# Kernel tuning notes

Hardware: AMD Instinct MI355X
Metric: run time of the kernel (lower is better)

The kernel has to match this reference:

```python
import jax, jax.numpy as jnp
import numpy as np

EPS = 1e-5

def _ln(x, s, b):
    m = jnp.mean(x, axis=-1, keepdims=True)
    v = jnp.mean((x - m) ** 2, axis=-1, keepdims=True)
    return (x - m) * jax.lax.rsqrt(v + EPS) * s + b

def _lin(x, w, b):
    # torch nn.Linear: y = x @ w.T + b, w shape (out, in)
    return jnp.einsum('...i,oi->...o', x, w) + b

def _gelu(x):
    return jax.nn.gelu(x, approximate=False)  # torch nn.GELU default (erf)

def setup_inputs() -> dict:
    key = jax.random.key(0)
    L, B, N, P, D, F, H = 4, 16, 8, 64, 128, 128, 8
    ks = jax.random.split(key, 16)
    nrm = lambda k, s: jax.random.normal(k, s, jnp.float32) * 0.02
    return {
        'sequence': jax.random.normal(ks[0], (B, N, P, D), jnp.float32),
        'H_pre': jax.random.normal(ks[1], (L, B, N, P, D), jnp.float32),
        'pro1_w': nrm(ks[2], (L, F, D)), 'pro1_b': jnp.zeros((L, F), jnp.float32),
        'pro2_w': nrm(ks[3], (L, F, D)), 'pro2_b': jnp.zeros((L, F), jnp.float32),
        'ln_cur_s': jnp.ones((L, F), jnp.float32), 'ln_cur_b': jnp.zeros((L, F), jnp.float32),
        'ln_pre_s': jnp.ones((L, F), jnp.float32), 'ln_pre_b': jnp.zeros((L, F), jnp.float32),
        'cur_qkv_w': nrm(ks[4], (L, 3 * H * F, F)), 'cur_qkv_b': jnp.zeros((L, 3 * H * F), jnp.float32),
        'pre_qkv_w': nrm(ks[5], (L, 3 * H * F, F)), 'pre_qkv_b': jnp.zeros((L, 3 * H * F), jnp.float32),
        'alpha': jax.random.uniform(ks[6], (L, 3, H * F), jnp.float32),
        'proj_w': nrm(ks[7], (L, F, H * F)), 'proj_b': jnp.zeros((L, F), jnp.float32),
        'bn1_s': jnp.ones((L, F), jnp.float32), 'bn1_b': jnp.zeros((L, F), jnp.float32),
        'bn2_s': jnp.ones((L, F), jnp.float32), 'bn2_b': jnp.zeros((L, F), jnp.float32),
        'ln_o_s': jnp.ones((L, F), jnp.float32), 'ln_o_b': jnp.zeros((L, F), jnp.float32),
        'ffn_w': nrm(ks[8], (L, F, F)), 'ffn_b': jnp.zeros((L, F), jnp.float32),
    }

def reference(sequence, H_pre, pro1_w, pro1_b, pro2_w, pro2_b, ln_cur_s, ln_cur_b,
              ln_pre_s, ln_pre_b, cur_qkv_w, cur_qkv_b, pre_qkv_w, pre_qkv_b, alpha,
              proj_w, proj_b, bn1_s, bn1_b, bn2_s, bn2_b, ln_o_s, ln_o_b, ffn_w, ffn_b):
    L = H_pre.shape[0]
    F = ffn_w.shape[-1]
    H = cur_qkv_w.shape[1] // (3 * F)
    scale = F ** -0.5  # Recur_self_attn: dim ** -0.5 with dim = ffn_dim

    def qkv(x, w, b):
        y = _lin(x, w, b)                      # (B, N, P, 3*H*F)
        Bq, Nq, Pq, _ = y.shape
        y = y.reshape(Bq, Nq, Pq, 3, H, F)     # matches 'b n (qkv h d)' split order
        y = jnp.transpose(y, (3, 0, 1, 4, 2, 5))  # (3, B, N, H, P, F)
        return y[0], y[1], y[2]

    cur = sequence  # (B, N, P, D); timesteps are independent in this module -> batched over N
    for l in range(L):
        if l == 0:  # only first cell sees last-dim == dim and projects cur
            cur = _ln(_lin(cur, pro1_w[l], pro1_b[l]), ln_cur_s[l], ln_cur_b[l])
        pre = _ln(_lin(H_pre[l], pro2_w[l], pro2_b[l]), ln_pre_s[l], ln_pre_b[l])

        Qc, Kc, Vc = qkv(cur, cur_qkv_w[l], cur_qkv_b[l])
        Qp, Kp, Vp = qkv(pre, pre_qkv_w[l], pre_qkv_b[l])
        a = jax.nn.sigmoid(alpha[l]).reshape(3, H, F)[:, None, None, :, None, :]  # (3,1,1,H,1,F)
        Q = a[0] * Qc + (1.0 - a[0]) * Qp
        K = a[1] * Kc + (1.0 - a[1]) * Kp
        V = a[2] * Vc + (1.0 - a[2]) * Vp

        attn = jax.nn.softmax(jnp.einsum('bnhpf,bnhqf->bnhpq', Q, K) * scale, axis=-1)
        A = jnp.einsum('bnhpq,bnhqf->bnhpf', attn, V)
        A = _ln(A, bn1_s[l], bn1_b[l])
        Bx, Nx, Hx, Px, Fx = A.shape
        A = jnp.transpose(A, (0, 1, 3, 2, 4)).reshape(Bx, Nx, Px, Hx * Fx)  # 'b h n d -> b n (h d)'
        A = _ln(_lin(A, proj_w[l], proj_b[l]), bn2_s[l], bn2_b[l])
        A = A + _gelu(cur)

        O_hat = _ln(cur + A, ln_o_s[l], ln_o_b[l])
        cur = _lin(O_hat, ffn_w[l], ffn_b[l]) + _gelu(O_hat)
    return cur
```

## Files before the change

### kernel.cpp

```cpp
#include <hip/hip_runtime.h>
#include <math.h>

#define EPS 1e-5f


typedef __bf16 bf16x8 __attribute__((ext_vector_type(8)));
typedef float f32x4 __attribute__((ext_vector_type(4)));

#define MFMA16 __builtin_amdgcn_mfma_f32_16x16x32_bf16

__device__ __forceinline__ float gelu_f(float x) {
    return 0.5f * x * (1.0f + erff(x * 0.7071067811865476f));
}

__device__ __forceinline__ void gll16(const void* g, void* l) {
    __builtin_amdgcn_global_load_lds(
        (const __attribute__((address_space(1))) void*)g,
        (__attribute__((address_space(3))) void*)l, 16, 0, 0);
}

__device__ __forceinline__ void cvt_store8(void* dst, const float* __restrict__ src) {
    float4 a = ((const float4*)src)[0];
    float4 b = ((const float4*)src)[1];
    bf16x8 v;
    v[0] = (__bf16)a.x; v[1] = (__bf16)a.y; v[2] = (__bf16)a.z; v[3] = (__bf16)a.w;
    v[4] = (__bf16)b.x; v[5] = (__bf16)b.y; v[6] = (__bf16)b.z; v[7] = (__bf16)b.w;
    *(bf16x8*)dst = v;
}

__device__ __forceinline__ int swz(int row, int k0)   { return row * 128 + (k0 ^ ((row & 7) << 3)); }
__device__ __forceinline__ int swz64(int row, int k0) { return row * 64  + (k0 ^ ((row & 7) << 3)); }

__global__ __launch_bounds__(256) void build_wq(
    const float* __restrict__ Wc, const float* __restrict__ bc,
    const float* __restrict__ Wp, const float* __restrict__ bp,
    const float* __restrict__ alpha,
    __bf16* __restrict__ Wq, float* __restrict__ bq)
{
    int idx = blockIdx.x * 256 + threadIdx.x;
    int l = idx / 98304, rem = idx - l * 98304;
    int row = rem >> 5, g = rem & 31, k0 = g << 3;
    float a = 1.0f / (1.0f + expf(-alpha[l * 3072 + row]));
    __bf16* dst = Wq + ((size_t)l * 3072 + row) * 256 + k0;
    if (k0 < 128) {
        const float* s = Wc + ((size_t)l * 3072 + row) * 128 + k0;
#pragma unroll
        for (int j = 0; j < 8; ++j) dst[j] = (__bf16)(a * s[j]);
    } else {
        const float* s = Wp + ((size_t)l * 3072 + row) * 128 + (k0 - 128);
#pragma unroll
        for (int j = 0; j < 8; ++j) dst[j] = (__bf16)((1.0f - a) * s[j]);
    }
    if (g == 0)
        bq[l * 3072 + row] = a * bc[l * 3072 + row] + (1.0f - a) * bp[l * 3072 + row];
}

__global__ __launch_bounds__(256) void cvt_all(
    const float* __restrict__ s0, __bf16* __restrict__ d0, int n0,
    const float* __restrict__ s1, __bf16* __restrict__ d1, int n1,
    const float* __restrict__ s2, __bf16* __restrict__ d2, int n2,
    const float* __restrict__ s3, __bf16* __restrict__ d3, int n3)
{
    int off = (blockIdx.x * 256 + threadIdx.x) * 4;
    const float* s; __bf16* d;
    if (off < n0) { s = s0; d = d0; }
    else {
        off -= n0;
        if (off < n1) { s = s1; d = d1; }
        else {
            off -= n1;
            if (off < n2) { s = s2; d = d2; }
            else {
                off -= n2;
                if (off >= n3) return;
                s = s3; d = d3;
            }
        }
    }
    float4 v = *(const float4*)(s + off);
    d[off] = (__bf16)v.x; d[off + 1] = (__bf16)v.y;
    d[off + 2] = (__bf16)v.z; d[off + 3] = (__bf16)v.w;
}

__global__ __launch_bounds__(256) void lin_pre_all(
    const float* __restrict__ Hpre, const __bf16* __restrict__ Wb,
    const float* __restrict__ bias, const float* __restrict__ lns_g,
    const float* __restrict__ lnb_g, __bf16* __restrict__ preb)
{
    __shared__ __align__(16) char lds[40960];
    unsigned short* xs = (unsigned short*)lds;
    unsigned short* ws = (unsigned short*)(lds + 8192);
    float* outs = (float*)lds;
    int l = blockIdx.x >> 8;
    int R = (blockIdx.x & 255) * 32;
    const float* x = Hpre + (size_t)l * 8192 * 128;
    const __bf16* Wbf = Wb + (size_t)l * 16384;
    const float* bias_l = bias + l * 128;
    const float* lns = lns_g + l * 128;
    const float* lnb = lnb_g + l * 128;
    __bf16* Xout = preb + (size_t)l * 8192 * 128;
    int t = threadIdx.x;
#pragma unroll
    for (int i = 0; i < 2; ++i) {
        int c = t + i * 256; int row = c >> 4, k0 = (c & 15) << 3;
        cvt_store8(&xs[swz(row, k0)], x + (size_t)(R + row) * 128 + k0);
    }
#pragma unroll
    for (int i = 0; i < 8; ++i) {
        int c = t + i * 256; int row = c >> 4, k0 = (c & 15) << 3;
        gll16(Wbf + (size_t)row * 128 + (k0 ^ ((row & 7) << 3)), &ws[c * 8]);
    }
    __syncthreads();
    int lane = t & 63, w = t >> 6;
    int wr = (w >> 1) * 16, wcol = (w & 1) * 64;
    int fr = lane & 15, fk = (lane >> 4) << 3;
    f32x4 acc[4] = {};
#pragma unroll
    for (int kk = 0; kk < 4; ++kk) {
        int k0 = kk * 32 + fk;
        bf16x8 a = *(const bf16x8*)&xs[swz(wr + fr, k0)];
#pragma unroll
        for (int n = 0; n < 4; ++n) {
            bf16x8 b = *(const bf16x8*)&ws[swz(wcol + n * 16 + fr, k0)];
            acc[n] = MFMA16(a, b, acc[n], 0, 0, 0);
        }
    }
    __syncthreads();
#pragma unroll
    for (int n = 0; n < 4; ++n) {
        int col = wcol + n * 16 + fr;
        float bv = bias_l[col];
        int rl = wr + ((lane >> 4) << 2);
#pragma unroll
        for (int r = 0; r < 4; ++r) outs[(rl + r) * 132 + col] = acc[n][r] + bv;
    }
    __syncthreads();
    int row = t >> 3, oc = t & 7;
    float vals[16]; float s = 0.0f;
#pragma unroll
    for (int i = 0; i < 16; ++i) { vals[i] = outs[row * 132 + oc + 8 * i]; s += vals[i]; }
    s += __shfl_xor(s, 1, 8); s += __shfl_xor(s, 2, 8); s += __shfl_xor(s, 4, 8);
    float mean = s * (1.0f / 128.0f);
    float sq = 0.0f;
#pragma unroll
    for (int i = 0; i < 16; ++i) { float d = vals[i] - mean; sq += d * d; }
    sq += __shfl_xor(sq, 1, 8); sq += __shfl_xor(sq, 2, 8); sq += __shfl_xor(sq, 4, 8);
    float rs = rsqrtf(sq * (1.0f / 128.0f) + EPS);
#pragma unroll
    for (int i = 0; i < 16; ++i) {
        int c = oc + 8 * i;
        Xout[(size_t)(R + row) * 128 + c] = (__bf16)((vals[i] - mean) * rs * lns[c] + lnb[c]);
    }
}

__global__ __launch_bounds__(256) void lin_ln_mfma(
    const float* __restrict__ x, const __bf16* __restrict__ Wbf,
    const float* __restrict__ bias, const float* __restrict__ lns,
    const float* __restrict__ lnb,
    float* __restrict__ yf, __bf16* __restrict__ Xout)
{
    __shared__ __align__(16) char lds[40960];
    unsigned short* xs = (unsigned short*)lds;
    unsigned short* ws = (unsigned short*)(lds + 8192);
    float* outs = (float*)lds;
    int t = threadIdx.x;
    int R = blockIdx.x * 32;
#pragma unroll
    for (int i = 0; i < 2; ++i) {
        int c = t + i * 256; int row = c >> 4, k0 = (c & 15) << 3;
        cvt_store8(&xs[swz(row, k0)], x + (size_t)(R + row) * 128 + k0);
    }
#pragma unroll
    for (int i = 0; i < 8; ++i) {
        int c = t + i * 256; int row = c >> 4, k0 = (c & 15) << 3;
        gll16(Wbf + (size_t)row * 128 + (k0 ^ ((row & 7) << 3)), &ws[c * 8]);
    }
    __syncthreads();
    int lane = t & 63, w = t >> 6;
    int wr = (w >> 1) * 16, wcol = (w & 1) * 64;
    int fr = lane & 15, fk = (lane >> 4) << 3;
    f32x4 acc[4] = {};
#pragma unroll
    for (int kk = 0; kk < 4; ++kk) {
        int k0 = kk * 32 + fk;
        bf16x8 a = *(const bf16x8*)&xs[swz(wr + fr, k0)];
#pragma unroll
        for (int n = 0; n < 4; ++n) {
            bf16x8 b = *(const bf16x8*)&ws[swz(wcol + n * 16 + fr, k0)];
            acc[n] = MFMA16(a, b, acc[n], 0, 0, 0);
        }
    }
    __syncthreads();
#pragma unroll
    for (int n = 0; n < 4; ++n) {
        int col = wcol + n * 16 + fr;
        float bv = bias[col];
        int rl = wr + ((lane >> 4) << 2);
#pragma unroll
        for (int r = 0; r < 4; ++r) outs[(rl + r) * 132 + col] = acc[n][r] + bv;
    }
    __syncthreads();
    int row = t >> 3, oc = t & 7;
    float vals[16]; float s = 0.0f;
#pragma unroll
    for (int i = 0; i < 16; ++i) { vals[i] = outs[row * 132 + oc + 8 * i]; s += vals[i]; }
    s += __shfl_xor(s, 1, 8); s += __shfl_xor(s, 2, 8); s += __shfl_xor(s, 4, 8);
    float mean = s * (1.0f / 128.0f);
    float sq = 0.0f;
#pragma unroll
    for (int i = 0; i < 16; ++i) { float d = vals[i] - mean; sq += d * d; }
    sq += __shfl_xor(sq, 1, 8); sq += __shfl_xor(sq, 2, 8); sq += __shfl_xor(sq, 4, 8);
    float rs = rsqrtf(sq * (1.0f / 128.0f) + EPS);
#pragma unroll
    for (int i = 0; i < 16; ++i) {
        int c = oc + 8 * i;
        float yv = (vals[i] - mean) * rs * lns[c] + lnb[c];
        yf[(size_t)(R + row) * 128 + c] = yv;
        Xout[(size_t)(R + row) * 128 + c] = (__bf16)yv;
    }
}

__global__ __launch_bounds__(256, 2) void qkv_attn(
    const __bf16* __restrict__ Xc, const __bf16* __restrict__ Pre,
    const __bf16* __restrict__ Wq, const float* __restrict__ bq,
    const float* __restrict__ bn1s, const float* __restrict__ bn1b,
    __bf16* __restrict__ At)
{
    __shared__ __align__(16) char lds[57344];
    unsigned short* As = (unsigned short*)lds;
    unsigned short* Bs = (unsigned short*)(lds + 8192);
    __bf16* Qs  = (__bf16*)lds;
    __bf16* Ks  = (__bf16*)(lds + 16384);
    __bf16* Vts = (__bf16*)(lds + 32768);
    __bf16* Ps  = (__bf16*)(lds + 49152);

    int bn = blockIdx.x >> 3, h = blockIdx.x & 7;
    int t = threadIdx.x, lane = t & 63, w = t >> 6;
    int fr = lane & 15, fk = (lane >> 4) << 3;
    int rr = (lane >> 4) << 2;
    int w16 = w * 16;

    f32x4 acc[24] = {};
    for (int kc = 0; kc < 4; ++kc) {
        const __bf16* xsrc = (kc < 2) ? Xc : Pre;
        int co = (kc & 1) * 64;
#pragma unroll
        for (int i = 0; i < 2; ++i) {
            int c = t + i * 256;
            int row = c >> 3, k0 = (c & 7) << 3;
            gll16(xsrc + (size_t)(bn * 64 + row) * 128 + co + (k0 ^ ((row & 7) << 3)),
                  &As[c * 8]);
        }
#pragma unroll
        for (int i = 0; i < 12; ++i) {
            int c = t + i * 256;
            int row = c >> 3, k0 = (c & 7) << 3;
            int type = row >> 7, f = row & 127;
            gll16(Wq + ((size_t)type * 1024 + h * 128 + f) * 256 + kc * 64 +
                      (k0 ^ ((row & 7) << 3)),
                  &Bs[c * 8]);
        }
        __syncthreads();
#pragma unroll
        for (int kk = 0; kk < 2; ++kk) {
            int k = kk * 32 + fk;
            int arow = w16 + fr;
            bf16x8 a = *(const bf16x8*)&As[arow * 64 + (k ^ ((arow & 7) << 3))];
#pragma unroll
            for (int n = 0; n < 24; ++n) {
                int j = n * 16 + fr;
                bf16x8 b = *(const bf16x8*)&Bs[j * 64 + (k ^ ((j & 7) << 3))];
                acc[n] = MFMA16(a, b, acc[n], 0, 0, 0);
            }
        }
        __syncthreads();
    }

#pragma unroll
    for (int n = 0; n < 24; ++n) {
        int type = n >> 3;
        int f = (n & 7) * 16 + fr;
        float bv = bq[type * 1024 + h * 128 + f];
#pragma unroll
        for (int r = 0; r < 4; ++r) {
            int row = w16 + rr + r;
            float val = acc[n][r] + bv;
            if (type == 0)
                Qs[row * 128 + (f ^ ((row & 7) << 3))] = (__bf16)val;
            else if (type == 1)
                Ks[row * 128 + (f ^ ((row & 7) << 3))] = (__bf16)val;
            else
                Vts[f * 64 + (row ^ ((f & 7) << 3))] = (__bf16)val;
        }
    }
    __syncthreads();

    f32x4 sacc[4] = {};
#pragma unroll
    for (int kk = 0; kk < 4; ++kk) {
        int k0 = kk * 32 + fk;
        int arow = w16 + fr;
        bf16x8 aq = *(const bf16x8*)&Qs[arow * 128 + (k0 ^ ((arow & 7) << 3))];
#pragma unroll
        for (int n = 0; n < 4; ++n) {
            bf16x8 bk = *(const bf16x8*)&Ks[swz(n * 16 + fr, k0)];
            sacc[n] = MFMA16(aq, bk, sacc[n], 0, 0, 0);
        }
    }

    const float scale = 0.08838834764831845f;
#pragma unroll
    for (int r = 0; r < 4; ++r) {
        float sv[4];
#pragma unroll
        for (int n = 0; n < 4; ++n) sv[n] = sacc[n][r] * scale;
        float mx = fmaxf(fmaxf(sv[0], sv[1]), fmaxf(sv[2], sv[3]));
        mx = fmaxf(mx, __shfl_xor(mx, 1, 16));
        mx = fmaxf(mx, __shfl_xor(mx, 2, 16));
        mx = fmaxf(mx, __shfl_xor(mx, 4, 16));
        mx = fmaxf(mx, __shfl_xor(mx, 8, 16));
        float sum = 0.0f;
#pragma unroll
        for (int n = 0; n < 4; ++n) { sv[n] = expf(sv[n] - mx); sum += sv[n]; }
        sum += __shfl_xor(sum, 1, 16);
        sum += __shfl_xor(sum, 2, 16);
        sum += __shfl_xor(sum, 4, 16);
        sum += __shfl_xor(sum, 8, 16);
        float inv = 1.0f / sum;
        int p = w16 + rr + r;
#pragma unroll
        for (int n = 0; n < 4; ++n) {
            int q = n * 16 + fr;
            Ps[p * 64 + (q ^ ((p & 7) << 3))] = (__bf16)(sv[n] * inv);
        }
    }
    __syncthreads();

    f32x4 oacc[8] = {};
#pragma unroll
    for (int kk = 0; kk < 2; ++kk) {
        int k0 = kk * 32 + fk;
        int arow = w16 + fr;
        bf16x8 ap = *(const bf16x8*)&Ps[arow * 64 + (k0 ^ ((arow & 7) << 3))];
#pragma unroll
        for (int n = 0; n < 8; ++n) {
            bf16x8 bv = *(const bf16x8*)&Vts[swz64(n * 16 + fr, k0)];
            oacc[n] = MFMA16(ap, bv, oacc[n], 0, 0, 0);
        }
    }

#pragma unroll
    for (int r = 0; r < 4; ++r) {
        int p = w16 + rr + r;
        float s1 = 0.0f;
#pragma unroll
        for (int n = 0; n < 8; ++n) s1 += oacc[n][r];
        s1 += __shfl_xor(s1, 1, 16);
        s1 += __shfl_xor(s1, 2, 16);
        s1 += __shfl_xor(s1, 4, 16);
        s1 += __shfl_xor(s1, 8, 16);
        float mean = s1 * (1.0f / 128.0f);
        float s2 = 0.0f;
#pragma unroll
        for (int n = 0; n < 8; ++n) { float d = oacc[n][r] - mean; s2 += d * d; }
        s2 += __shfl_xor(s2, 1, 16);
        s2 += __shfl_xor(s2, 2, 16);
        s2 += __shfl_xor(s2, 4, 16);
        s2 += __shfl_xor(s2, 8, 16);
        float rs = rsqrtf(s2 * (1.0f / 128.0f) + EPS);
        __bf16* orow = At + (size_t)(bn * 64 + p) * 1024 + h * 128;
#pragma unroll
        for (int n = 0; n < 8; ++n) {
            int f = n * 16 + fr;
            orow[f] = (__bf16)((oacc[n][r] - mean) * rs * bn1s[f] + bn1b[f]);
        }
    }
}

__global__ __launch_bounds__(256) void proj_ffn_mfma(
    const __bf16* __restrict__ At_g, const __bf16* __restrict__ Wp,
    const float* __restrict__ pb,
    const float* __restrict__ bn2s, const float* __restrict__ bn2b,
    const float* __restrict__ lnos, const float* __restrict__ lnob,
    const __bf16* __restrict__ Wf, const float* __restrict__ fb,
    const float* __restrict__ cur, float* __restrict__ out,
    __bf16* __restrict__ Xcur)
{
    __shared__ __align__(16) char lds[40960];
    unsigned short* ats = (unsigned short*)lds;
    unsigned short* wts = (unsigned short*)(lds + 8192);
    float* outs = (float*)lds;
    int t = threadIdx.x;
    int R = blockIdx.x * 32;
    int lane = t & 63, w = t >> 6;
    int wr = (w >> 1) * 16, wcol = (w & 1) * 64;
    int fr = lane & 15, fk = (lane >> 4) << 3;

    f32x4 acc[4] = {};
    for (int kc = 0; kc < 8; ++kc) {
#pragma unroll
        for (int i = 0; i < 2; ++i) {
            int c = t + i * 256; int row = c >> 4, k0 = (c & 15) << 3;
            gll16(At_g + (size_t)(R + row) * 1024 + kc * 128 + (k0 ^ ((row & 7) << 3)),
                  &ats[c * 8]);
        }
#pragma unroll
        for (int i = 0; i < 8; ++i) {
            int c = t + i * 256; int row = c >> 4, k0 = (c & 15) << 3;
            gll16(Wp + (size_t)row * 1024 + kc * 128 + (k0 ^ ((row & 7) << 3)),
                  &wts[c * 8]);
        }
        __syncthreads();
#pragma unroll
        for (int kk = 0; kk < 4; ++kk) {
            int k0 = kk * 32 + fk;
            bf16x8 a = *(const bf16x8*)&ats[swz(wr + fr, k0)];
#pragma unroll
            for (int n = 0; n < 4; ++n) {
                bf16x8 b = *(const bf16x8*)&wts[swz(wcol + n * 16 + fr, k0)];
                acc[n] = MFMA16(a, b, acc[n], 0, 0, 0);
            }
        }
        __syncthreads();
    }

#pragma unroll
    for (int n = 0; n < 4; ++n) {
        int col = wcol + n * 16 + fr;
        float bv = pb[col];
        int rl = wr + ((lane >> 4) << 2);
#pragma unroll
        for (int r = 0; r < 4; ++r) outs[(rl + r) * 132 + col] = acc[n][r] + bv;
    }
    __syncthreads();

    int row = t >> 3, oc = t & 7;
    float vals[16]; float s = 0.0f;
#pragma unroll
    for (int i = 0; i < 16; ++i) { vals[i] = outs[row * 132 + oc + 8 * i]; s += vals[i]; }
    s += __shfl_xor(s, 1, 8); s += __shfl_xor(s, 2, 8); s += __shfl_xor(s, 4, 8);
    float mean = s * (1.0f / 128.0f);
    float sq = 0.0f;
#pragma unroll
    for (int i = 0; i < 16; ++i) { float d = vals[i] - mean; sq += d * d; }
    sq += __shfl_xor(sq, 1, 8); sq += __shfl_xor(sq, 2, 8); sq += __shfl_xor(sq, 4, 8);
    float rs = rsqrtf(sq * (1.0f / 128.0f) + EPS);

    float oh[16]; float s2 = 0.0f;
#pragma unroll
    for (int i = 0; i < 16; ++i) {
        int c = oc + 8 * i;
        float ynorm = (vals[i] - mean) * rs * bn2s[c] + bn2b[c];
        float cv = cur[(size_t)(R + row) * 128 + c];
        oh[i] = cv + (ynorm + gelu_f(cv));
        s2 += oh[i];
    }
    s2 += __shfl_xor(s2, 1, 8); s2 += __shfl_xor(s2, 2, 8); s2 += __shfl_xor(s2, 4, 8);
    float mean2 = s2 * (1.0f / 128.0f);
    float sq2 = 0.0f;
#pragma unroll
    for (int i = 0; i < 16; ++i) { float d = oh[i] - mean2; sq2 += d * d; }
    sq2 += __shfl_xor(sq2, 1, 8); sq2 += __shfl_xor(sq2, 2, 8); sq2 += __shfl_xor(sq2, 4, 8);
    float rs2 = rsqrtf(sq2 * (1.0f / 128.0f) + EPS);
#pragma unroll
    for (int i = 0; i < 16; ++i) {
        int c = oc + 8 * i;
        oh[i] = (oh[i] - mean2) * rs2 * lnos[c] + lnob[c];
    }
    __syncthreads();

#pragma unroll
    for (int i = 0; i < 16; ++i) {
        int c = oc + 8 * i;
        ((__bf16*)ats)[row * 128 + (c ^ ((row & 7) << 3))] = (__bf16)oh[i];
    }
#pragma unroll
    for (int i = 0; i < 8; ++i) {
        int c = t + i * 256; int rw = c >> 4, k0 = (c & 15) << 3;
        gll16(Wf + (size_t)rw * 128 + (k0 ^ ((rw & 7) << 3)), &wts[c * 8]);
    }
    __syncthreads();

    f32x4 acc2[4] = {};
#pragma unroll
    for (int kk = 0; kk < 4; ++kk) {
        int k0 = kk * 32 + fk;
        bf16x8 a = *(const bf16x8*)&ats[swz(wr + fr, k0)];
#pragma unroll
        for (int n = 0; n < 4; ++n) {
            bf16x8 b = *(const bf16x8*)&wts[swz(wcol + n * 16 + fr, k0)];
            acc2[n] = MFMA16(a, b, acc2[n], 0, 0, 0);
        }
    }
#pragma unroll
    for (int n = 0; n < 4; ++n) {
        int col = wcol + n * 16 + fr;
        float bv = fb[col];
#pragma unroll
        for (int r = 0; r < 4; ++r) {
            int ro = wr + ((lane >> 4) << 2) + r;
            float ov = (float)((__bf16*)ats)[ro * 128 + (col ^ ((ro & 7) << 3))];
            float val = acc2[n][r] + bv + gelu_f(ov);
            size_t gidx = (size_t)(R + ro) * 128 + col;
            out[gidx] = val;
            if (Xcur) Xcur[gidx] = (__bf16)val;
        }
    }
}

extern "C" void kernel_launch(void* const* d_in, const int* in_sizes, int n_in,
                              void* d_out, int out_size, void* d_ws, size_t ws_size,
                              hipStream_t stream)
{
    const float* seq       = (const float*)d_in[0];
    const float* Hpre      = (const float*)d_in[1];
    const float* pro1_w    = (const float*)d_in[2];
    const float* pro1_b    = (const float*)d_in[3];
    const float* pro2_w    = (const float*)d_in[4];
    const float* pro2_b    = (const float*)d_in[5];
    const float* ln_cur_s  = (const float*)d_in[6];
    const float* ln_cur_b  = (const float*)d_in[7];
    const float* ln_pre_s  = (const float*)d_in[8];
    const float* ln_pre_b  = (const float*)d_in[9];
    const float* cur_qkv_w = (const float*)d_in[10];
    const float* cur_qkv_b = (const float*)d_in[11];
    const float* pre_qkv_w = (const float*)d_in[12];
    const float* pre_qkv_b = (const float*)d_in[13];
    const float* alpha     = (const float*)d_in[14];
    const float* proj_w    = (const float*)d_in[15];
    const float* proj_b    = (const float*)d_in[16];
    const float* bn1_s     = (const float*)d_in[17];
    const float* bn1_b     = (const float*)d_in[18];
    const float* bn2_s     = (const float*)d_in[19];
    const float* bn2_b     = (const float*)d_in[20];
    const float* ln_o_s    = (const float*)d_in[21];
    const float* ln_o_b    = (const float*)d_in[22];
    const float* ffn_w     = (const float*)d_in[23];
    const float* ffn_b     = (const float*)d_in[24];

    char* ws = (char*)d_ws;
    __bf16* Wq      = (__bf16*)ws;                 ws += (size_t)4 * 3072 * 256 * 2;
    float*  bq      = (float*)ws;                  ws += (size_t)4 * 3072 * 4;
    __bf16* Wp_bf   = (__bf16*)ws;                 ws += (size_t)4 * 128 * 1024 * 2;
    __bf16* Wf_bf   = (__bf16*)ws;                 ws += (size_t)4 * 128 * 128 * 2;
    __bf16* pro1_bf = (__bf16*)ws;                 ws += (size_t)128 * 128 * 2;
    __bf16* pro2_bf = (__bf16*)ws;                 ws += (size_t)4 * 128 * 128 * 2;
    __bf16* Xc   = (__bf16*)ws;                    ws += (size_t)8192 * 128 * 2;
    __bf16* preb = (__bf16*)ws;                    ws += (size_t)4 * 8192 * 128 * 2;
    float*  cur  = (float*)ws;                     ws += (size_t)8192 * 128 * 4;
    __bf16* Atb  = (__bf16*)ws;                    ws += (size_t)8192 * 1024 * 2;

    build_wq<<<1536, 256, 0, stream>>>(cur_qkv_w, cur_qkv_b, pre_qkv_w, pre_qkv_b,
                                       alpha, Wq, bq);
    cvt_all<<<656, 256, 0, stream>>>(proj_w, Wp_bf, 4 * 128 * 1024,
                                     ffn_w, Wf_bf, 4 * 128 * 128,
                                     pro1_w, pro1_bf, 128 * 128,
                                     pro2_w, pro2_bf, 4 * 128 * 128);
    lin_pre_all<<<1024, 256, 0, stream>>>(Hpre, pro2_bf, pro2_b,
                                          ln_pre_s, ln_pre_b, preb);
    lin_ln_mfma<<<256, 256, 0, stream>>>(seq, pro1_bf, pro1_b,
                                         ln_cur_s, ln_cur_b, cur, Xc);

    for (int l = 0; l < 4; ++l) {
        qkv_attn<<<1024, 256, 0, stream>>>(
            Xc, preb + (size_t)l * 8192 * 128,
            Wq + (size_t)l * 3072 * 256, bq + l * 3072,
            bn1_s + l * 128, bn1_b + l * 128, Atb);
        float* outp = (l == 3) ? (float*)d_out : cur;
        proj_ffn_mfma<<<256, 256, 0, stream>>>(Atb,
                                               Wp_bf + (size_t)l * 128 * 1024,
                                               proj_b + l * 128,
                                               bn2_s + l * 128, bn2_b + l * 128,
                                               ln_o_s + l * 128, ln_o_b + l * 128,
                                               Wf_bf + (size_t)l * 16384,
                                               ffn_b + l * 128,
                                               cur, outp, (l == 3) ? nullptr : Xc);
    }
}
```

Measured before the change: 235.5 us.

## Retile QKV GEMM per-wave column split and halve proj_ffn row tile

The fused QKV weight matrix is reordered so each head's Q/K/V rows are contiguous. In qkv_attn each wave now computes all 64 rows times a 96-column slice instead of 16 rows times 384 columns, cutting redundant B-fragment LDS reads in favour of reused A fragments, at the cost of more accumulator registers. proj_ffn_mfma now processes 16 rows per block with 512 blocks to improve occupancy and CU coverage, though each block reloads the full weight tiles, increasing total weight traffic.

```diff
diff --git a/kernel.cpp b/kernel.cpp
--- a/kernel.cpp
+++ b/kernel.cpp
@@ -40,8 +40,10 @@
     int idx = blockIdx.x * 256 + threadIdx.x;
     int l = idx / 98304, rem = idx - l * 98304;
     int row = rem >> 5, g = rem & 31, k0 = g << 3;
+    int type = row >> 10, hf = row & 1023, h = hf >> 7, f = hf & 127;
+    int rowp = h * 384 + type * 128 + f;
     float a = 1.0f / (1.0f + expf(-alpha[l * 3072 + row]));
-    __bf16* dst = Wq + ((size_t)l * 3072 + row) * 256 + k0;
+    __bf16* dst = Wq + ((size_t)l * 3072 + rowp) * 256 + k0;
     if (k0 < 128) {
         const float* s = Wc + ((size_t)l * 3072 + row) * 128 + k0;
 #pragma unroll
@@ -52,7 +54,7 @@
         for (int j = 0; j < 8; ++j) dst[j] = (__bf16)((1.0f - a) * s[j]);
     }
     if (g == 0)
-        bq[l * 3072 + row] = a * bc[l * 3072 + row] + (1.0f - a) * bp[l * 3072 + row];
+        bq[l * 3072 + rowp] = a * bc[l * 3072 + row] + (1.0f - a) * bp[l * 3072 + row];
 }
 
 __global__ __launch_bounds__(256) void cvt_all(
@@ -239,8 +241,10 @@
     int fr = lane & 15, fk = (lane >> 4) << 3;
     int rr = (lane >> 4) << 2;
     int w16 = w * 16;
-
-    f32x4 acc[24] = {};
+    const __bf16* Wqh = Wq + (size_t)h * 384 * 256;
+    const float* bqh = bq + h * 384;
+
+    f32x4 acc[4][6] = {};
     for (int kc = 0; kc < 4; ++kc) {
         const __bf16* xsrc = (kc < 2) ? Xc : Pre;
         int co = (kc & 1) * 64;
@@ -255,42 +259,52 @@
         for (int i = 0; i < 12; ++i) {
             int c = t + i * 256;
             int row = c >> 3, k0 = (c & 7) << 3;
-            int type = row >> 7, f = row & 127;
-            gll16(Wq + ((size_t)type * 1024 + h * 128 + f) * 256 + kc * 64 +
-                      (k0 ^ ((row & 7) << 3)),
+            gll16(Wqh + (size_t)row * 256 + kc * 64 + (k0 ^ ((row & 7) << 3)),
                   &Bs[c * 8]);
         }
         __syncthreads();
 #pragma unroll
         for (int kk = 0; kk < 2; ++kk) {
             int k = kk * 32 + fk;
-            int arow = w16 + fr;
-            bf16x8 a = *(const bf16x8*)&As[arow * 64 + (k ^ ((arow & 7) << 3))];
-#pragma unroll
-            for (int n = 0; n < 24; ++n) {
-                int j = n * 16 + fr;
-                bf16x8 b = *(const bf16x8*)&Bs[j * 64 + (k ^ ((j & 7) << 3))];
-                acc[n] = MFMA16(a, b, acc[n], 0, 0, 0);
+            bf16x8 a[4], b[6];
+#pragma unroll
+            for (int m = 0; m < 4; ++m) {
+                int r = m * 16 + fr;
+                a[m] = *(const bf16x8*)&As[r * 64 + (k ^ ((r & 7) << 3))];
             }
+#pragma unroll
+            for (int n = 0; n < 6; ++n) {
+                int j = w * 96 + n * 16 + fr;
+                b[n] = *(const bf16x8*)&Bs[j * 64 + (k ^ ((j & 7) << 3))];
+            }
+#pragma unroll
+            for (int m = 0; m < 4; ++m)
+#pragma unroll
+                for (int n = 0; n < 6; ++n)
+                    acc[m][n] = MFMA16(a[m], b[n], acc[m][n], 0, 0, 0);
         }
         __syncthreads();
     }
 
 #pragma unroll
-    for (int n = 0; n < 24; ++n) {
-        int type = n >> 3;
-        int f = (n & 7) * 16 + fr;
-        float bv = bq[type * 1024 + h * 128 + f];
-#pragma unroll
-        for (int r = 0; r < 4; ++r) {
-            int row = w16 + rr + r;
-            float val = acc[n][r] + bv;
-            if (type == 0)
-                Qs[row * 128 + (f ^ ((row & 7) << 3))] = (__bf16)val;
-            else if (type == 1)
-                Ks[row * 128 + (f ^ ((row & 7) << 3))] = (__bf16)val;
-            else
-                Vts[f * 64 + (row ^ ((f & 7) << 3))] = (__bf16)val;
+    for (int n = 0; n < 6; ++n) {
+        int colb = w * 96 + n * 16;
+        int type = colb >> 7;
+        float bv = bqh[colb + fr];
+        int f = (colb & 127) + fr;
+#pragma unroll
+        for (int m = 0; m < 4; ++m) {
+#pragma unroll
+            for (int r = 0; r < 4; ++r) {
+                int row = m * 16 + rr + r;
+                float val = acc[m][n][r] + bv;
+                if (type == 0)
+                    Qs[row * 128 + (f ^ ((row & 7) << 3))] = (__bf16)val;
+                else if (type == 1)
+                    Ks[row * 128 + (f ^ ((row & 7) << 3))] = (__bf16)val;
+                else
+                    Vts[f * 64 + (row ^ ((f & 7) << 3))] = (__bf16)val;
+            }
         }
     }
     __syncthreads();
@@ -386,23 +400,23 @@
     const float* __restrict__ cur, float* __restrict__ out,
     __bf16* __restrict__ Xcur)
 {
-    __shared__ __align__(16) char lds[40960];
+    __shared__ __align__(16) char lds[36864];
     unsigned short* ats = (unsigned short*)lds;
-    unsigned short* wts = (unsigned short*)(lds + 8192);
+    unsigned short* wts = (unsigned short*)(lds + 4096);
     float* outs = (float*)lds;
     int t = threadIdx.x;
-    int R = blockIdx.x * 32;
+    int R = blockIdx.x * 16;
     int lane = t & 63, w = t >> 6;
-    int wr = (w >> 1) * 16, wcol = (w & 1) * 64;
+    int wcol = w * 32;
     int fr = lane & 15, fk = (lane >> 4) << 3;
-
-    f32x4 acc[4] = {};
+    int rr = (lane >> 4) << 2;
+
+    f32x4 acc[2] = {};
     for (int kc = 0; kc < 8; ++kc) {
-#pragma unroll
-        for (int i = 0; i < 2; ++i) {
-            int c = t + i * 256; int row = c >> 4, k0 = (c & 15) << 3;
+        {
+            int row = t >> 4, k0 = (t & 15) << 3;
             gll16(At_g + (size_t)(R + row) * 1024 + kc * 128 + (k0 ^ ((row & 7) << 3)),
-                  &ats[c * 8]);
+                  &ats[t * 8]);
         }
 #pragma unroll
         for (int i = 0; i < 8; ++i) {
@@ -414,9 +428,9 @@
 #pragma unroll
         for (int kk = 0; kk < 4; ++kk) {
             int k0 = kk * 32 + fk;
-            bf16x8 a = *(const bf16x8*)&ats[swz(wr + fr, k0)];
-#pragma unroll
-            for (int n = 0; n < 4; ++n) {
+            bf16x8 a = *(const bf16x8*)&ats[swz(fr, k0)];
+#pragma unroll
+            for (int n = 0; n < 2; ++n) {
                 bf16x8 b = *(const bf16x8*)&wts[swz(wcol + n * 16 + fr, k0)];
                 acc[n] = MFMA16(a, b, acc[n], 0, 0, 0);
             }
@@ -425,53 +439,56 @@
     }
 
 #pragma unroll
-    for (int n = 0; n < 4; ++n) {
+    for (int n = 0; n < 2; ++n) {
         int col = wcol + n * 16 + fr;
         float bv = pb[col];
-        int rl = wr + ((lane >> 4) << 2);
-#pragma unroll
-        for (int r = 0; r < 4; ++r) outs[(rl + r) * 132 + col] = acc[n][r] + bv;
-    }
-    __syncthreads();
-
-    int row = t >> 3, oc = t & 7;
-    float vals[16]; float s = 0.0f;
-#pragma unroll
-    for (int i = 0; i < 16; ++i) { vals[i] = outs[row * 132 + oc + 8 * i]; s += vals[i]; }
-    s += __shfl_xor(s, 1, 8); s += __shfl_xor(s, 2, 8); s += __shfl_xor(s, 4, 8);
+#pragma unroll
+        for (int r = 0; r < 4; ++r) outs[(rr + r) * 132 + col] = acc[n][r] + bv;
+    }
+    __syncthreads();
+
+    int row = t >> 4, oc = t & 15;
+    float vals[8]; float s = 0.0f;
+#pragma unroll
+    for (int i = 0; i < 8; ++i) { vals[i] = outs[row * 132 + oc + 16 * i]; s += vals[i]; }
+    s += __shfl_xor(s, 1, 16); s += __shfl_xor(s, 2, 16);
+    s += __shfl_xor(s, 4, 16); s += __shfl_xor(s, 8, 16);
     float mean = s * (1.0f / 128.0f);
     float sq = 0.0f;
 #pragma unroll
-    for (int i = 0; i < 16; ++i) { float d = vals[i] - mean; sq += d * d; }
-    sq += __shfl_xor(sq, 1, 8); sq += __shfl_xor(sq, 2, 8); sq += __shfl_xor(sq, 4, 8);
+    for (int i = 0; i < 8; ++i) { float d = vals[i] - mean; sq += d * d; }
+    sq += __shfl_xor(sq, 1, 16); sq += __shfl_xor(sq, 2, 16);
+    sq += __shfl_xor(sq, 4, 16); sq += __shfl_xor(sq, 8, 16);
     float rs = rsqrtf(sq * (1.0f / 128.0f) + EPS);
 
-    float oh[16]; float s2 = 0.0f;
-#pragma unroll
-    for (int i = 0; i < 16; ++i) {
-        int c = oc + 8 * i;
+    float oh[8]; float s2 = 0.0f;
+#pragma unroll
+    for (int i = 0; i < 8; ++i) {
+        int c = oc + 16 * i;
         float ynorm = (vals[i] - mean) * rs * bn2s[c] + bn2b[c];
         float cv = cur[(size_t)(R + row) * 128 + c];
         oh[i] = cv + (ynorm + gelu_f(cv));
         s2 += oh[i];
     }
-    s2 += __shfl_xor(s2, 1, 8); s2 += __shfl_xor(s2, 2, 8); s2 += __shfl_xor(s2, 4, 8);
+    s2 += __shfl_xor(s2, 1, 16); s2 += __shfl_xor(s2, 2, 16);
+    s2 += __shfl_xor(s2, 4, 16); s2 += __shfl_xor(s2, 8, 16);
     float mean2 = s2 * (1.0f / 128.0f);
     float sq2 = 0.0f;
 #pragma unroll
-    for (int i = 0; i < 16; ++i) { float d = oh[i] - mean2; sq2 += d * d; }
-    sq2 += __shfl_xor(sq2, 1, 8); sq2 += __shfl_xor(sq2, 2, 8); sq2 += __shfl_xor(sq2, 4, 8);
+    for (int i = 0; i < 8; ++i) { float d = oh[i] - mean2; sq2 += d * d; }
+    sq2 += __shfl_xor(sq2, 1, 16); sq2 += __shfl_xor(sq2, 2, 16);
+    sq2 += __shfl_xor(sq2, 4, 16); sq2 += __shfl_xor(sq2, 8, 16);
     float rs2 = rsqrtf(sq2 * (1.0f / 128.0f) + EPS);
 #pragma unroll
-    for (int i = 0; i < 16; ++i) {
-        int c = oc + 8 * i;
+    for (int i = 0; i < 8; ++i) {
+        int c = oc + 16 * i;
         oh[i] = (oh[i] - mean2) * rs2 * lnos[c] + lnob[c];
     }
     __syncthreads();
 
 #pragma unroll
-    for (int i = 0; i < 16; ++i) {
-        int c = oc + 8 * i;
+    for (int i = 0; i < 8; ++i) {
+        int c = oc + 16 * i;
         ((__bf16*)ats)[row * 128 + (c ^ ((row & 7) << 3))] = (__bf16)oh[i];
     }
 #pragma unroll
@@ -481,24 +498,24 @@
     }
     __syncthreads();
 
-    f32x4 acc2[4] = {};
+    f32x4 acc2[2] = {};
 #pragma unroll
     for (int kk = 0; kk < 4; ++kk) {
         int k0 = kk * 32 + fk;
-        bf16x8 a = *(const bf16x8*)&ats[swz(wr + fr, k0)];
-#pragma unroll
-        for (int n = 0; n < 4; ++n) {
+        bf16x8 a = *(const bf16x8*)&ats[swz(fr, k0)];
+#pragma unroll
+        for (int n = 0; n < 2; ++n) {
             bf16x8 b = *(const bf16x8*)&wts[swz(wcol + n * 16 + fr, k0)];
             acc2[n] = MFMA16(a, b, acc2[n], 0, 0, 0);
         }
     }
 #pragma unroll
-    for (int n = 0; n < 4; ++n) {
+    for (int n = 0; n < 2; ++n) {
         int col = wcol + n * 16 + fr;
         float bv = fb[col];
 #pragma unroll
         for (int r = 0; r < 4; ++r) {
-            int ro = wr + ((lane >> 4) << 2) + r;
+            int ro = rr + r;
             float ov = (float)((__bf16*)ats)[ro * 128 + (col ^ ((ro & 7) << 3))];
             float val = acc2[n][r] + bv + gelu_f(ov);
             size_t gidx = (size_t)(R + ro) * 128 + col;
@@ -567,7 +584,7 @@
             Wq + (size_t)l * 3072 * 256, bq + l * 3072,
             bn1_s + l * 128, bn1_b + l * 128, Atb);
         float* outp = (l == 3) ? (float*)d_out : cur;
-        proj_ffn_mfma<<<256, 256, 0, stream>>>(Atb,
+        proj_ffn_mfma<<<512, 256, 0, stream>>>(Atb,
                                                Wp_bf + (size_t)l * 128 * 1024,
                                                proj_b + l * 128,
                                                bn2_s + l * 128, bn2_b + l * 128,
```

Result: no change. 238.7 us (+1.4%).
